# Kernel tuning notes

Measured on AMD Instinct MI355X. Metric: run time of the kernel, lower is better.

Reference implementation:

```python
import jax, jax.numpy as jnp
import numpy as np

B = 1024      # batch size
T = 32        # num_tables
D = 64        # embedding_dim
E = 100000    # num_embeddings (rows per table)
L = 50        # pooling factor (indices per bag)


def setup_inputs() -> dict:
    key = jax.random.key(0)
    kw, ki = jax.random.split(key)
    embedding_weights = jax.random.normal(kw, (E, T, D), dtype=jnp.float32)
    sharded_sparse_features = jax.random.randint(ki, (B * T * L,), 0, E, dtype=jnp.int32)
    # uniform-length bags: offsets[i] = i * L, length B*T + 1
    sharded_offsets = jnp.arange(B * T + 1, dtype=jnp.int32) * L
    return {
        "embedding_weights": embedding_weights,
        "sharded_sparse_features": sharded_sparse_features,
        "sharded_offsets": sharded_offsets,
    }


def reference(embedding_weights, sharded_sparse_features, sharded_offsets):
    # Table-batched embedding-bag with sum pooling.
    # embedding_weights: [E, T, D]; indices: [N]; offsets: [B*T + 1]
    # bag j pools indices[offsets[j]:offsets[j+1]] from table (j % T).
    N = sharded_sparse_features.shape[0]
    num_bags = sharded_offsets.shape[0] - 1  # B * T
    # bag id for each flat index position
    seg = jnp.searchsorted(sharded_offsets, jnp.arange(N, dtype=sharded_offsets.dtype), side="right") - 1
    table = seg % T  # which table each index reads from
    rows = embedding_weights[sharded_sparse_features, table, :]  # [N, D]
    pooled = jax.ops.segment_sum(rows, seg, num_segments=num_bags)  # [B*T, D]
    return pooled.reshape(B, T, D)
```

## Files before the change

kernel.cpp:

```cpp
#include <hip/hip_runtime.h>


constexpr int kT = 32;
constexpr int kD = 64;

__global__ __launch_bounds__(256) void embag_kernel(
    const float* __restrict__ weights,
    const int*   __restrict__ features,
    const int*   __restrict__ offsets,
    float*       __restrict__ out,
    int num_bags)
{
    const int gwave = (int)((blockIdx.x * 256u + threadIdx.x) >> 6);
    const int lane  = (int)(threadIdx.x & 63u);
    if (gwave >= num_bags) return;

    const int bag = gwave;
    const int t   = bag & (kT - 1);
    const float* wb = weights + (size_t)t * kD + lane;
    const size_t row_stride = (size_t)kT * kD;

    const int start = offsets[bag];
    const int end   = offsets[bag + 1];

    float a0 = 0.f, a1 = 0.f;
    int n = start;
    #pragma unroll 4
    for (; n + 2 <= end; n += 2) {
        const int e0 = features[n];
        const int e1 = features[n + 1];
        a0 += wb[(size_t)e0 * row_stride];
        a1 += wb[(size_t)e1 * row_stride];
    }
    if (n < end) {
        const int e0 = features[n];
        a0 += wb[(size_t)e0 * row_stride];
    }
    out[(size_t)bag * kD + lane] = a0 + a1;
}

extern "C" void kernel_launch(void* const* d_in, const int* in_sizes, int n_in,
                              void* d_out, int out_size, void* d_ws, size_t ws_size,
                              hipStream_t stream) {
    const float* weights  = (const float*)d_in[0];
    const int*   features = (const int*)d_in[1];
    const int*   offsets  = (const int*)d_in[2];
    float*       out      = (float*)d_out;

    const int num_bags = in_sizes[2] - 1;
    const int threads  = 256;
    const int waves    = num_bags;
    const int blocks   = (waves * 64 + threads - 1) / threads;

    embag_kernel<<<blocks, threads, 0, stream>>>(weights, features, offsets, out, num_bags);
}
```

Baseline: 938.5 us.

## Vectorize row gathers with float4 across 4 rows per wave and regroup bags by table

Each wave now reads four embedding rows at once with float4 loads (16 lanes per row), loads all bag indices in one coalesced load, broadcasts them with shuffles, and reduces the partial sums across lane groups. Bags are remapped so consecutive waves work on the same table. A fully unrolled path for bags of length 50 has 13 independent loads in flight. The aim is higher memory-level parallelism and fewer load instructions for random row gathers. The cost is an extra cross-lane reduction and wasted lanes on the last iteration.

```diff
diff --git a/kernel.cpp b/kernel.cpp
--- a/kernel.cpp
+++ b/kernel.cpp
@@ -3,6 +3,7 @@
 
 constexpr int kT = 32;
 constexpr int kD = 64;
+constexpr int kL = 50;
 
 __global__ __launch_bounds__(256) void embag_kernel(
     const float* __restrict__ weights,
@@ -15,28 +16,70 @@
     const int lane  = (int)(threadIdx.x & 63u);
     if (gwave >= num_bags) return;
 
-    const int bag = gwave;
-    const int t   = bag & (kT - 1);
-    const float* wb = weights + (size_t)t * kD + lane;
-    const size_t row_stride = (size_t)kT * kD;
+    int bag = gwave;
+    if ((num_bags & (kT - 1)) == 0) {
+        const int groups = num_bags >> 5;
+        bag = (gwave % groups) * kT + (gwave / groups);
+    }
 
+    const int t     = bag & (kT - 1);
     const int start = offsets[bag];
     const int end   = offsets[bag + 1];
+    const int count = end - start;
 
-    float a0 = 0.f, a1 = 0.f;
-    int n = start;
-    #pragma unroll 4
-    for (; n + 2 <= end; n += 2) {
-        const int e0 = features[n];
-        const int e1 = features[n + 1];
-        a0 += wb[(size_t)e0 * row_stride];
-        a1 += wb[(size_t)e1 * row_stride];
+    const int r = lane >> 4;
+    const int c = lane & 15;
+
+    const float*  wbase      = weights + (size_t)t * kD + (size_t)(c * 4);
+    const size_t  row_stride = (size_t)kT * kD;
+
+    float4 acc0 = make_float4(0.f, 0.f, 0.f, 0.f);
+    float4 acc1 = make_float4(0.f, 0.f, 0.f, 0.f);
+
+    if (count == kL) {
+        const int idx = features[start + (lane < kL ? lane : kL - 1)];
+
+        #pragma unroll
+        for (int k = 0; k < 13; ++k) {
+            const int row = k * 4 + r;
+            const int e   = __shfl(idx, row < kL ? row : (kL - 1), 64);
+            const float4 v = *(const float4*)(wbase + (size_t)e * row_stride);
+            const float  s = (row < kL) ? 1.0f : 0.0f;
+            if (k & 1) {
+                acc1.x = fmaf(v.x, s, acc1.x);
+                acc1.y = fmaf(v.y, s, acc1.y);
+                acc1.z = fmaf(v.z, s, acc1.z);
+                acc1.w = fmaf(v.w, s, acc1.w);
+            } else {
+                acc0.x = fmaf(v.x, s, acc0.x);
+                acc0.y = fmaf(v.y, s, acc0.y);
+                acc0.z = fmaf(v.z, s, acc0.z);
+                acc0.w = fmaf(v.w, s, acc0.w);
+            }
+        }
+    } else {
+        for (int n = start + r; n < end; n += 4) {
+            const int e = features[n];
+            const float4 v = *(const float4*)(wbase + (size_t)e * row_stride);
+            acc0.x += v.x; acc0.y += v.y; acc0.z += v.z; acc0.w += v.w;
+        }
     }
-    if (n < end) {
-        const int e0 = features[n];
-        a0 += wb[(size_t)e0 * row_stride];
+
+    float4 acc = make_float4(acc0.x + acc1.x, acc0.y + acc1.y,
+                             acc0.z + acc1.z, acc0.w + acc1.w);
+
+    acc.x += __shfl_xor(acc.x, 16, 64);
+    acc.y += __shfl_xor(acc.y, 16, 64);
+    acc.z += __shfl_xor(acc.z, 16, 64);
+    acc.w += __shfl_xor(acc.w, 16, 64);
+    acc.x += __shfl_xor(acc.x, 32, 64);
+    acc.y += __shfl_xor(acc.y, 32, 64);
+    acc.z += __shfl_xor(acc.z, 32, 64);
+    acc.w += __shfl_xor(acc.w, 32, 64);
+
+    if (r == 0) {
+        *(float4*)(out + (size_t)bag * kD + (size_t)(c * 4)) = acc;
     }
-    out[(size_t)bag * kD + lane] = a0 + a1;
 }
 
 extern "C" void kernel_launch(void* const* d_in, const int* in_sizes, int n_in,
```

New measurement: 939.0 us. Within noise of the previous version (+0.0%).

## Bin lookups by embedding row and sweep rows with atomic accumulation

Applied to the files above, without the earlier changes.

Replaces the per-bag gather with a three-phase scheme: zero the output and per-row cursors, bin each lookup's bag id into per-row buckets, then sweep each embedding row once and atomically add its table slices into the target bags. The aim is to turn scattered row gathers into row-grouped reads with better DRAM locality. It adds a workspace requirement, many float atomics on the output, overflow handling via per-element atomics, and nondeterministic summation order. The original kernel remains as a fallback when the workspace is too small.

```diff
diff --git a/kernel.cpp b/kernel.cpp
--- a/kernel.cpp
+++ b/kernel.cpp
@@ -1,8 +1,95 @@
 #include <hip/hip_runtime.h>
 
 
-constexpr int kT = 32;
-constexpr int kD = 64;
+constexpr int kT   = 32;
+constexpr int kD   = 64;
+constexpr int kCap = 64;
+
+__global__ __launch_bounds__(256) void zero_kernel(
+    int* __restrict__ cursors, int E,
+    float* __restrict__ out, int out_elems)
+{
+    const int i      = blockIdx.x * 256 + threadIdx.x;
+    const int stride = gridDim.x * 256;
+    for (int k = i; k < E; k += stride) cursors[k] = 0;
+    for (int k = i; k < out_elems; k += stride) out[k] = 0.f;
+}
+
+__global__ __launch_bounds__(256) void bin_kernel(
+    const float* __restrict__ weights,
+    const int*   __restrict__ features,
+    const int*   __restrict__ offsets,
+    int*            __restrict__ cursors,
+    unsigned short* __restrict__ buckets,
+    float*          __restrict__ out,
+    int num_bags)
+{
+    const int gwave = (int)((blockIdx.x * 256u + threadIdx.x) >> 6);
+    const int lane  = (int)(threadIdx.x & 63u);
+    if (gwave >= num_bags) return;
+
+    const int bag   = gwave;
+    const int start = offsets[bag];
+    const int end   = offsets[bag + 1];
+
+    for (int n = start + lane; n < end; n += 64) {
+        const int e    = features[n];
+        const int slot = atomicAdd(&cursors[e], 1);
+        if (slot < kCap) {
+            buckets[(size_t)e * kCap + slot] = (unsigned short)bag;
+        } else {
+            const int t = bag & (kT - 1);
+            const float* w = weights + (size_t)e * (kT * kD) + (size_t)t * kD;
+            float* o = out + (size_t)bag * kD;
+            for (int d = 0; d < kD; ++d) {
+                __hip_atomic_fetch_add(&o[d], w[d],
+                    __ATOMIC_RELAXED, __HIP_MEMORY_SCOPE_AGENT);
+            }
+        }
+    }
+}
+
+__global__ __launch_bounds__(256) void sweep_kernel(
+    const float* __restrict__ weights,
+    const int*            __restrict__ cursors,
+    const unsigned short* __restrict__ buckets,
+    float* __restrict__ out,
+    int E)
+{
+    const int gwave = (int)((blockIdx.x * 256u + threadIdx.x) >> 6);
+    const int lane  = (int)(threadIdx.x & 63u);
+    if (gwave >= E) return;
+
+    const int e = gwave;
+    int cnt = cursors[e];
+    cnt = cnt < kCap ? cnt : kCap;
+    if (cnt == 0) return;
+
+    const int my = (lane < cnt) ? (int)buckets[(size_t)e * kCap + lane] : 0;
+
+    const float* wbase = weights + (size_t)e * (kT * kD) + lane;
+
+    int j = 0;
+    for (; j + 2 <= cnt; j += 2) {
+        const int bag0 = __shfl(my, j, 64);
+        const int bag1 = __shfl(my, j + 1, 64);
+        const int t0 = bag0 & (kT - 1);
+        const int t1 = bag1 & (kT - 1);
+        const float v0 = wbase[t0 * kD];
+        const float v1 = wbase[t1 * kD];
+        __hip_atomic_fetch_add(out + (size_t)bag0 * kD + lane, v0,
+            __ATOMIC_RELAXED, __HIP_MEMORY_SCOPE_AGENT);
+        __hip_atomic_fetch_add(out + (size_t)bag1 * kD + lane, v1,
+            __ATOMIC_RELAXED, __HIP_MEMORY_SCOPE_AGENT);
+    }
+    if (j < cnt) {
+        const int bag0 = __shfl(my, j, 64);
+        const int t0 = bag0 & (kT - 1);
+        const float v0 = wbase[t0 * kD];
+        __hip_atomic_fetch_add(out + (size_t)bag0 * kD + lane, v0,
+            __ATOMIC_RELAXED, __HIP_MEMORY_SCOPE_AGENT);
+    }
+}
 
 __global__ __launch_bounds__(256) void embag_kernel(
     const float* __restrict__ weights,
@@ -33,8 +120,7 @@
         a1 += wb[(size_t)e1 * row_stride];
     }
     if (n < end) {
-        const int e0 = features[n];
-        a0 += wb[(size_t)e0 * row_stride];
+        a0 += wb[(size_t)features[n] * row_stride];
     }
     out[(size_t)bag * kD + lane] = a0 + a1;
 }
@@ -48,9 +134,34 @@
     float*       out      = (float*)d_out;
 
     const int num_bags = in_sizes[2] - 1;
-    const int threads  = 256;
-    const int waves    = num_bags;
-    const int blocks   = (waves * 64 + threads - 1) / threads;
+    const int E        = in_sizes[0] / (kT * kD);
 
-    embag_kernel<<<blocks, threads, 0, stream>>>(weights, features, offsets, out, num_bags);
+    const size_t cur_bytes = ((size_t)E * sizeof(int) + 511) & ~(size_t)511;
+    const size_t bkt_bytes = (size_t)E * kCap * sizeof(unsigned short);
+    const size_t need      = cur_bytes + bkt_bytes;
+
+    const bool binned_ok =
+        d_ws != nullptr && ws_size >= need &&
+        num_bags > 0 && num_bags <= 65536 &&
+        (size_t)E * (kT * kD) == (size_t)in_sizes[0];
+
+    if (binned_ok) {
+        int* cursors = (int*)d_ws;
+        unsigned short* buckets = (unsigned short*)((char*)d_ws + cur_bytes);
+        const int out_elems = num_bags * kD;
+
+        zero_kernel<<<2048, 256, 0, stream>>>(cursors, E, out, out_elems);
+
+        const int bin_blocks = (num_bags * 64 + 255) / 256;
+        bin_kernel<<<bin_blocks, 256, 0, stream>>>(
+            weights, features, offsets, cursors, buckets, out, num_bags);
+
+        const int sweep_blocks = (E * 64 + 255) / 256;
+        sweep_kernel<<<sweep_blocks, 256, 0, stream>>>(
+            weights, cursors, buckets, out, E);
+    } else {
+        const int blocks = (num_bags * 64 + 255) / 256;
+        embag_kernel<<<blocks, 256, 0, stream>>>(
+            weights, features, offsets, out, num_bags);
+    }
 }
```

Measured after the change: 1.290 ms. +37.4%, slower.
